# Kernel optimization log

Measured on AMD Instinct MI355X. Metric: run time of the kernel, lower is better.

## Reference

```python
import jax, jax.numpy as jnp
import numpy as np

T = 40          # self.T / timestep
T_REDUCE = 32
FAC = T_REDUCE / T - 0.001  # 0.799, threshold used by create_spike_input_cuda


def conv_t(x, w, b, pad):
    # x: (N,C,H,W,T); w: (O,I,3,3). SLAYER/catSNN conv = Conv3d with time-kernel 1,
    # i.e. the same 2D conv applied independently at every timestep.
    out = jax.lax.conv_general_dilated(
        x, w[..., None], window_strides=(1, 1, 1),
        padding=[(pad, pad), (pad, pad), (0, 0)],
        dimension_numbers=("NCHWT", "OIHWT", "NCHWT"))
    return out + b[None, :, None, None, None]


def avgpool2(x):
    # 2x2 spatial average pool per timestep (snn.pool(2))
    N, C, H, W, Tt = x.shape
    return x.reshape(N, C, H // 2, 2, W // 2, 2, Tt).mean(axis=(3, 5))


def get_spikes(x, thr):
    # catCuda.getSpikes: integrate-and-fire over the last (time) axis with
    # soft reset (subtract threshold). thr broadcastable to x[..., 0].
    xT = jnp.moveaxis(x, -1, 0)                      # (T, N, C, H, W)
    thr_b = jnp.broadcast_to(jnp.asarray(thr, x.dtype), xT.shape[1:])
    def step(v, xt):
        v = v + xt
        s = (v >= thr_b).astype(x.dtype)
        return v - s * thr_b, s
    _, s = jax.lax.scan(step, jnp.zeros(xT.shape[1:], x.dtype), xT)
    return jnp.moveaxis(s, 0, -1)


def requant(y):
    # create_spike_input_cuda(sum(y, time)/T, T): stack the time-mean T times
    # and spike-generate with threshold FAC.
    ym = jnp.mean(y, axis=-1)                        # sum over time / T
    yb = jnp.broadcast_to(ym[..., None], ym.shape + (T,))
    return get_spikes(yb, FAC)


def tts(xi, yi, thr):
    # threshold_training_snn: per-channel spiking of xi, requantized copy of yi.
    return get_spikes(xi, thr[None, :, None, None]), requant(yi)


def forward(x, thr1, thr2, thr3, thr4, thr5, thr6, thr7, p1, p2, p3, p4,
            w1, b1, w2, b2, w3, b3, w4, b4, w5, b5, w6, b6, w7, b7, wc, bc):
    c = conv_t(x, w1, b1, 1)
    xs, ys = tts(c, c, thr1)
    xs, ys = tts(conv_t(xs, w2, b2, 1), conv_t(ys, w2, b2, 1), thr2)
    xs, ys = tts(avgpool2(xs), avgpool2(ys), p1)
    xs, ys = tts(conv_t(xs, w3, b3, 1), conv_t(ys, w3, b3, 1), thr3)
    xs, ys = tts(conv_t(xs, w4, b4, 1), conv_t(ys, w4, b4, 1), thr4)
    xs, ys = tts(avgpool2(xs), avgpool2(ys), p2)
    xs, ys = tts(conv_t(xs, w5, b5, 1), conv_t(ys, w5, b5, 1), thr5)
    xs, ys = tts(conv_t(xs, w6, b6, 1), conv_t(ys, w6, b6, 1), thr6)
    xs, ys = tts(avgpool2(xs), avgpool2(ys), p3)
    xs, ys = tts(conv_t(xs, w7, b7, 0), conv_t(ys, w7, b7, 0), thr7)
    xs, ys = tts(avgpool2(xs), avgpool2(ys), p4)
    N = xs.shape[0]
    xr = xs.reshape(N, 1024, T)                      # spatial is 1x1 here
    logits = jnp.einsum("nct,oc->not", xr, wc) + bc[None, :, None]
    out = jnp.sum(logits, axis=-1) / T               # sum_spikes / T
    return out.reshape(N, 10, 1, 1)


def setup_inputs() -> dict:
    key = jax.random.key(0)
    ks = jax.random.split(key, 32)
    inp = {}
    inp["x"] = jax.random.uniform(ks[0], (2, 3, 32, 32, T), jnp.float32)
    chans = [(3, 128), (128, 128), (128, 256), (256, 256),
             (256, 512), (512, 512), (512, 1024)]
    for i, (ci, co) in enumerate(chans, 1):
        inp[f"w{i}"] = jax.random.normal(ks[i], (co, ci, 3, 3), jnp.float32) * (2.0 / (ci * 9)) ** 0.5
        inp[f"b{i}"] = jnp.zeros((co,), jnp.float32)
    inp["wc"] = jax.random.normal(ks[8], (10, 1024), jnp.float32) * 0.03
    inp["bc"] = jnp.zeros((10,), jnp.float32)
    thr_dims = {"thr1": 128, "thr2": 128, "p1": 128, "thr3": 256, "thr4": 256,
                "p2": 256, "thr5": 512, "thr6": 512, "p3": 512, "thr7": 1024, "p4": 1024}
    for j, (name, d) in enumerate(thr_dims.items()):
        inp[name] = 0.2 + jax.random.uniform(ks[9 + j], (d,), jnp.float32)
    return inp


def reference(x, thr1, thr2, thr3, thr4, thr5, thr6, thr7, p1, p2, p3, p4,
              w1, b1, w2, b2, w3, b3, w4, b4, w5, b5, w6, b6, w7, b7, wc, bc):
    return forward(x, thr1, thr2, thr3, thr4, thr5, thr6, thr7, p1, p2, p3, p4,
                   w1, b1, w2, b2, w3, b3, w4, b4, w5, b5, w6, b6, w7, b7, wc, bc)
```

## Files before the change

kernel.cpp:

```cpp
#include <hip/hip_runtime.h>


constexpr int NT = 40;

typedef __attribute__((ext_vector_type(8))) short s16x8;
typedef __attribute__((ext_vector_type(4))) float f32x4;

__device__ __forceinline__ float bf2f(unsigned short u) {
    return __uint_as_float(((unsigned)u) << 16);
}

__global__ __launch_bounds__(256) void transpose_w(
    const float* __restrict__ w, float* __restrict__ wt, int CO, int R)
{
    __shared__ float tile[32][33];
    const int r0 = blockIdx.x * 32, c0 = blockIdx.y * 32;
    const int tx = threadIdx.x % 32, ty = threadIdx.x / 32;
#pragma unroll
    for (int k = 0; k < 4; k++) {
        const int co = c0 + ty + k * 8, r = r0 + tx;
        if (co < CO && r < R) tile[ty + k * 8][tx] = w[(size_t)co * R + r];
    }
    __syncthreads();
#pragma unroll
    for (int k = 0; k < 4; k++) {
        const int r = r0 + ty + k * 8, co = c0 + tx;
        if (r < R && co < CO) wt[(size_t)r * CO + co] = tile[tx][ty + k * 8];
    }
}

__global__ __launch_bounds__(320) void conv1_c(
    const float* __restrict__ in, const float* __restrict__ wt,
    const float* __restrict__ bias, float* __restrict__ out)
{
    __shared__ float xs_[27 * NT];
    __shared__ float wl[27 * 128];
    const int sp = blockIdx.x;
    const int ho = sp >> 5, wo = sp & 31;
    const int n = blockIdx.z;
    const int tid = threadIdx.x;
    const int tt = tid >> 5;
    const int cc = tid & 31;

    float4 acc[4];
#pragma unroll
    for (int j = 0; j < 4; j++) {
        const float bv = bias[cc * 4 + j];
        acc[j] = make_float4(bv, bv, bv, bv);
    }
    for (int u = tid; u < 270; u += 320) {
        const int r = u / 10, q = u % 10;
        const int cil = r / 9, k = r % 9;
        const int hi = ho + k / 3 - 1, wi = wo + k % 3 - 1;
        float4 v = make_float4(0.f, 0.f, 0.f, 0.f);
        if ((unsigned)hi < 32u && (unsigned)wi < 32u)
            v = *reinterpret_cast<const float4*>(
                in + ((size_t)((n * 3 + cil) * 1024 + hi * 32 + wi)) * NT + q * 4);
        *reinterpret_cast<float4*>(&xs_[r * NT + q * 4]) = v;
    }
    for (int u = tid; u < 864; u += 320) {
        const int r = u >> 5, j = u & 31;
        *reinterpret_cast<float4*>(&wl[r * 128 + j * 4]) =
            *reinterpret_cast<const float4*>(wt + r * 128 + j * 4);
    }
    __syncthreads();
#pragma unroll
    for (int r = 0; r < 27; ++r) {
        const float4 xv = *reinterpret_cast<const float4*>(&xs_[r * NT + tt * 4]);
        const float4 wv = *reinterpret_cast<const float4*>(&wl[r * 128 + cc * 4]);
        acc[0].x = fmaf(xv.x, wv.x, acc[0].x); acc[0].y = fmaf(xv.y, wv.x, acc[0].y);
        acc[0].z = fmaf(xv.z, wv.x, acc[0].z); acc[0].w = fmaf(xv.w, wv.x, acc[0].w);
        acc[1].x = fmaf(xv.x, wv.y, acc[1].x); acc[1].y = fmaf(xv.y, wv.y, acc[1].y);
        acc[1].z = fmaf(xv.z, wv.y, acc[1].z); acc[1].w = fmaf(xv.w, wv.y, acc[1].w);
        acc[2].x = fmaf(xv.x, wv.z, acc[2].x); acc[2].y = fmaf(xv.y, wv.z, acc[2].y);
        acc[2].z = fmaf(xv.z, wv.z, acc[2].z); acc[2].w = fmaf(xv.w, wv.z, acc[2].w);
        acc[3].x = fmaf(xv.x, wv.w, acc[3].x); acc[3].y = fmaf(xv.y, wv.w, acc[3].y);
        acc[3].z = fmaf(xv.z, wv.w, acc[3].z); acc[3].w = fmaf(xv.w, wv.w, acc[3].w);
    }
    const size_t base = (size_t)(n * 1024 + sp) * (NT * 128);
#pragma unroll
    for (int j = 0; j < 4; j++) {
        const int cb = cc * 4 + j;
        out[base + (tt * 4 + 0) * 128 + cb] = acc[j].x;
        out[base + (tt * 4 + 1) * 128 + cb] = acc[j].y;
        out[base + (tt * 4 + 2) * 128 + cb] = acc[j].z;
        out[base + (tt * 4 + 3) * 128 + cb] = acc[j].w;
    }
}

__global__ void split_w(const float* __restrict__ w,
                        unsigned short* __restrict__ hi, unsigned short* __restrict__ mid,
                        unsigned short* __restrict__ lo, int CO, int CIN_)
{
    const int idx = blockIdx.x * blockDim.x + threadIdx.x;
    if (idx >= CO * CIN_) return;
    const int co = idx / CIN_, ci = idx % CIN_;
    const float* src = w + ((size_t)co * CIN_ + ci) * 9;
#pragma unroll
    for (int k = 0; k < 9; ++k) {
        const float f = src[k];
        const unsigned u = __float_as_uint(f);
        const float fh = __uint_as_float(u & 0xFFFF0000u);
        const float r1 = f - fh;
        const unsigned u1 = __float_as_uint(r1);
        const float fm = __uint_as_float(u1 & 0xFFFF0000u);
        const float r2 = r1 - fm;
        const unsigned u2 = __float_as_uint(r2);
        const size_t dst = ((size_t)k * CO + co) * CIN_ + ci;
        hi[dst] = (unsigned short)(u >> 16);
        mid[dst] = (unsigned short)(u1 >> 16);
        lo[dst] = (unsigned short)(u2 >> 16);
    }
}

template<int CIN_SEG, int COUT, int H, int W, int PAD, int BM, int BN, int NSPLIT>
__global__ __launch_bounds__(256, 2) void conv_mfma(
    const unsigned short* __restrict__ spk,
    const unsigned short* __restrict__ wlo, const unsigned short* __restrict__ wmid,
    const unsigned short* __restrict__ whi,
    const float* __restrict__ bias, float* __restrict__ out)
{
    constexpr int CIN = CIN_SEG * NSPLIT;
    constexpr int HO = PAD ? H : H - 2;
    constexpr int WO = PAD ? W : W - 2;
    constexpr int MROW = WO * NT;
    constexpr int MTILES = (MROW + BM - 1) / BM;
    constexpr int WAVES_N = BN / 32;
    constexpr int KC = CIN_SEG / 64;
    __shared__ unsigned short smem[BM * 64 + 3 * BN * 64];

    const int tid = threadIdx.x;
    const int lane = tid & 63;
    const int wv = tid >> 6;
    const int wm = wv / WAVES_N;
    const int wn = wv % WAVES_N;
    const int lr = lane >> 4;
    const int lc = lane & 15;

    const int bx = blockIdx.x;
    const int ho = bx / MTILES;
    const int m0 = (bx % MTILES) * BM;
    const int co0 = blockIdx.y * BN;
    const int n = blockIdx.z / NSPLIT;
    const int split = blockIdx.z % NSPLIT;

    f32x4 acc[4][2];
#pragma unroll
    for (int mf = 0; mf < 4; ++mf)
#pragma unroll
        for (int nf = 0; nf < 2; ++nf) {
            const float bv = (NSPLIT == 1 || split == 0)
                ? bias[co0 + wn * 32 + nf * 16 + lc] : 0.f;
            acc[mf][nf] = {bv, bv, bv, bv};
        }

    const unsigned short* wp[3] = {wlo, wmid, whi};

    for (int kh = 0; kh < 3; ++kh) {
        const int hirow = ho + kh - PAD;
        if (hirow < 0 || hirow >= H) continue;
        const size_t inrow = (size_t)(n * H + hirow) * (W * NT);
        for (int kw = 0; kw < 3; ++kw) {
            const int kwp = kw - PAD;
            const int khw = kh * 3 + kw;
            for (int kc = 0; kc < KC; ++kc) {
                const int ci0 = split * CIN_SEG + kc * 64;
#pragma unroll
                for (int it = 0; it < BM / 32; ++it) {
                    const int idx = it * 256 + tid;
                    const int r = idx >> 3, b = idx & 7;
                    const int mg = m0 + r + kwp * NT;
                    s16x8 v = {0, 0, 0, 0, 0, 0, 0, 0};
                    if ((m0 + r) < MROW && mg >= 0 && mg < W * NT)
                        v = *(const s16x8*)(spk + (inrow + mg) * CIN + ci0 + b * 8);
                    *(s16x8*)&smem[r * 64 + ((b ^ (r & 7)) << 3)] = v;
                }
#pragma unroll
                for (int s = 0; s < 3; ++s) {
                    const unsigned short* wsrc = wp[s] + ((size_t)(khw * COUT + co0)) * CIN + ci0;
#pragma unroll
                    for (int it = 0; it < BN / 32; ++it) {
                        const int idx = it * 256 + tid;
                        const int r = idx >> 3, b = idx & 7;
                        const s16x8 v = *(const s16x8*)(wsrc + (size_t)r * CIN + b * 8);
                        *(s16x8*)&smem[BM * 64 + s * BN * 64 + r * 64 + ((b ^ (r & 7)) << 3)] = v;
                    }
                }
                __syncthreads();
#pragma unroll
                for (int kcs = 0; kcs < 2; ++kcs) {
                    const int c16 = kcs * 4 + lr;
                    s16x8 af[4];
#pragma unroll
                    for (int mf = 0; mf < 4; ++mf) {
                        const int ra = wm * 64 + mf * 16 + lc;
                        af[mf] = *(const s16x8*)&smem[ra * 64 + ((c16 ^ (ra & 7)) << 3)];
                    }
#pragma unroll
                    for (int s = 0; s < 3; ++s) {
#pragma unroll
                        for (int nf = 0; nf < 2; ++nf) {
                            const int rb = wn * 32 + nf * 16 + lc;
                            const s16x8 bf_ = *(const s16x8*)&smem[BM * 64 + s * BN * 64 + rb * 64 + ((c16 ^ (rb & 7)) << 3)];
#pragma unroll
                            for (int mf = 0; mf < 4; ++mf)
                                acc[mf][nf] = __builtin_amdgcn_mfma_f32_16x16x32_bf16(
                                    af[mf], bf_, acc[mf][nf], 0, 0, 0);
                        }
                    }
                }
                __syncthreads();
            }
        }
    }

    const size_t SLAB = (size_t)2 * HO * WO * NT * COUT;
    float* outp = out + (size_t)split * SLAB + (size_t)(n * HO + ho) * (WO * NT) * COUT;
#pragma unroll
    for (int mf = 0; mf < 4; ++mf) {
        const int mbase = m0 + wm * 64 + mf * 16;
        if (mbase >= MROW) continue;
#pragma unroll
        for (int nf = 0; nf < 2; ++nf) {
            const int col = co0 + wn * 32 + nf * 16 + lc;
#pragma unroll
            for (int j = 0; j < 4; ++j) {
                const int m = mbase + lr * 4 + j;
                outp[(size_t)m * COUT + col] = acc[mf][nf][j];
            }
        }
    }
}

__global__ void if_ci(const float* __restrict__ in, unsigned short* __restrict__ spk,
                      const float* __restrict__ thr, int C, int total)
{
    const int idx = blockIdx.x * blockDim.x + threadIdx.x;
    if (idx >= total) return;
    const int c = idx % C;
    const size_t base = (size_t)(idx / C) * NT * C + c;
    const float th = thr[c];
    float v = 0.f;
#pragma unroll
    for (int t = 0; t < NT; ++t) {
        const float x = in[base + (size_t)t * C];
        v += x;
        const float s = (v >= th) ? 1.f : 0.f;
        v -= s * th;
        spk[base + (size_t)t * C] = s != 0.f ? (unsigned short)0x3F80 : (unsigned short)0;
    }
}

__global__ void pool_ci(const unsigned short* __restrict__ in, unsigned short* __restrict__ out,
                        const float* __restrict__ thr, int C, int HO, int WO, int total)
{
    const int idx = blockIdx.x * blockDim.x + threadIdx.x;
    if (idx >= total) return;
    const int c = idx % C;
    const int sp = idx / C;
    const int wo = sp % WO;
    const int ho = (sp / WO) % HO;
    const int n = sp / (WO * HO);
    const int H = 2 * HO, W = 2 * WO;
    const size_t b00 = (((size_t)(n * H + 2 * ho) * W + 2 * wo) * NT) * C + c;
    const size_t oB = (((size_t)(n * HO + ho) * WO + wo) * NT) * C + c;
    const size_t dW = (size_t)NT * C, dH = (size_t)W * NT * C;
    const float th = thr[c];
    float v = 0.f;
#pragma unroll
    for (int t = 0; t < NT; ++t) {
        const size_t o = (size_t)t * C;
        const float a = bf2f(in[b00 + o]) + bf2f(in[b00 + dW + o]) +
                        bf2f(in[b00 + dH + o]) + bf2f(in[b00 + dH + dW + o]);
        v += a * 0.25f;
        const float s = (v >= th) ? 1.f : 0.f;
        v -= s * th;
        out[oB + o] = s != 0.f ? (unsigned short)0x3F80 : (unsigned short)0;
    }
}

__global__ void reduce_if7(const float* __restrict__ part, unsigned short* __restrict__ out,
                           const float* __restrict__ thr, int total)
{
    const int idx = blockIdx.x * blockDim.x + threadIdx.x;
    if (idx >= total) return;
    const int c = idx & 1023;
    const size_t base = (size_t)(idx >> 10) * NT * 1024 + c;
    const size_t SL = 327680;
    const float th = thr[c];
    float v = 0.f;
#pragma unroll
    for (int t = 0; t < NT; ++t) {
        const size_t o = (size_t)t * 1024;
        const float x = part[base + o] + part[SL + base + o] +
                        part[2 * SL + base + o] + part[3 * SL + base + o];
        v += x;
        const float s = (v >= th) ? 1.f : 0.f;
        v -= s * th;
        out[base + o] = s != 0.f ? (unsigned short)0x3F80 : (unsigned short)0;
    }
}

__global__ __launch_bounds__(1024) void classifier_ci(
    const unsigned short* __restrict__ s, const float* __restrict__ wc,
    const float* __restrict__ bc, float* __restrict__ out)
{
    __shared__ float cnt[2][1024];
    const int c = threadIdx.x;
    for (int n = 0; n < 2; n++) {
        float sum = 0.f;
#pragma unroll
        for (int t = 0; t < NT; ++t) sum += bf2f(s[(size_t)(n * NT + t) * 1024 + c]);
        cnt[n][c] = sum;
    }
    __syncthreads();
    if (threadIdx.x < 20) {
        const int n = threadIdx.x / 10, o = threadIdx.x % 10;
        float a = 0.f;
        for (int k = 0; k < 1024; k++) a += cnt[n][k] * wc[o * 1024 + k];
        out[n * 10 + o] = a * (1.f / 40.f) + bc[o];
    }
}

extern "C" void kernel_launch(void* const* d_in, const int* in_sizes, int n_in,
                              void* d_out, int out_size, void* d_ws, size_t ws_size,
                              hipStream_t stream)
{
    const float* x   = (const float*)d_in[0];
    const float* w1  = (const float*)d_in[1];  const float* b1 = (const float*)d_in[2];
    const float* w2  = (const float*)d_in[3];  const float* b2 = (const float*)d_in[4];
    const float* w3  = (const float*)d_in[5];  const float* b3 = (const float*)d_in[6];
    const float* w4  = (const float*)d_in[7];  const float* b4 = (const float*)d_in[8];
    const float* w5  = (const float*)d_in[9];  const float* b5 = (const float*)d_in[10];
    const float* w6  = (const float*)d_in[11]; const float* b6 = (const float*)d_in[12];
    const float* w7  = (const float*)d_in[13]; const float* b7 = (const float*)d_in[14];
    const float* wc  = (const float*)d_in[15]; const float* bc = (const float*)d_in[16];
    const float* thr1 = (const float*)d_in[17];
    const float* thr2 = (const float*)d_in[18];
    const float* p1   = (const float*)d_in[19];
    const float* thr3 = (const float*)d_in[20];
    const float* thr4 = (const float*)d_in[21];
    const float* p2   = (const float*)d_in[22];
    const float* thr5 = (const float*)d_in[23];
    const float* thr6 = (const float*)d_in[24];
    const float* p3   = (const float*)d_in[25];
    const float* thr7 = (const float*)d_in[26];
    const float* p4   = (const float*)d_in[27];

    char* W0 = (char*)d_ws;
    float* OUT = (float*)W0;
    unsigned short* SPKA = (unsigned short*)(W0 + ((size_t)44 << 20));
    unsigned short* SPKB = (unsigned short*)(W0 + ((size_t)66 << 20));
    unsigned short* WH   = (unsigned short*)(W0 + ((size_t)88 << 20));
    unsigned short* WMID = WH + 4718592;
    unsigned short* WLO  = WH + 2 * 4718592;
    float* WT1 = (float*)(W0 + ((size_t)118 << 20));
    float* O = (float*)d_out;

    transpose_w<<<dim3(1, 4), 256, 0, stream>>>(w1, WT1, 128, 27);
    conv1_c<<<dim3(1024, 1, 2), 320, 0, stream>>>(x, WT1, b1, OUT);
    if_ci<<<1024, 256, 0, stream>>>(OUT, SPKA, thr1, 128, 262144);

    split_w<<<64, 256, 0, stream>>>(w2, WH, WMID, WLO, 128, 128);
    conv_mfma<128, 128, 32, 32, 1, 128, 64, 1><<<dim3(320, 2, 2), 256, 0, stream>>>(SPKA, WLO, WMID, WH, b2, OUT);
    if_ci<<<1024, 256, 0, stream>>>(OUT, SPKB, thr2, 128, 262144);
    pool_ci<<<256, 256, 0, stream>>>(SPKB, SPKA, p1, 128, 16, 16, 65536);

    split_w<<<128, 256, 0, stream>>>(w3, WH, WMID, WLO, 256, 128);
    conv_mfma<128, 256, 16, 16, 1, 128, 64, 1><<<dim3(80, 4, 2), 256, 0, stream>>>(SPKA, WLO, WMID, WH, b3, OUT);
    if_ci<<<512, 256, 0, stream>>>(OUT, SPKB, thr3, 256, 131072);

    split_w<<<256, 256, 0, stream>>>(w4, WH, WMID, WLO, 256, 256);
    conv_mfma<256, 256, 16, 16, 1, 128, 64, 1><<<dim3(80, 4, 2), 256, 0, stream>>>(SPKB, WLO, WMID, WH, b4, OUT);
    if_ci<<<512, 256, 0, stream>>>(OUT, SPKA, thr4, 256, 131072);
    pool_ci<<<128, 256, 0, stream>>>(SPKA, SPKB, p2, 256, 8, 8, 32768);

    split_w<<<512, 256, 0, stream>>>(w5, WH, WMID, WLO, 512, 256);
    conv_mfma<256, 512, 8, 8, 1, 64, 128, 1><<<dim3(40, 4, 2), 256, 0, stream>>>(SPKB, WLO, WMID, WH, b5, OUT);
    if_ci<<<256, 256, 0, stream>>>(OUT, SPKA, thr5, 512, 65536);

    split_w<<<1024, 256, 0, stream>>>(w6, WH, WMID, WLO, 512, 512);
    conv_mfma<512, 512, 8, 8, 1, 64, 128, 1><<<dim3(40, 4, 2), 256, 0, stream>>>(SPKA, WLO, WMID, WH, b6, OUT);
    if_ci<<<256, 256, 0, stream>>>(OUT, SPKB, thr6, 512, 65536);
    pool_ci<<<64, 256, 0, stream>>>(SPKB, SPKA, p3, 512, 4, 4, 16384);

    split_w<<<2048, 256, 0, stream>>>(w7, WH, WMID, WLO, 1024, 512);
    conv_mfma<128, 1024, 4, 4, 0, 64, 128, 4><<<dim3(4, 8, 8), 256, 0, stream>>>(SPKA, WLO, WMID, WH, b7, OUT);
    reduce_if7<<<32, 256, 0, stream>>>(OUT, SPKB, thr7, 8192);
    pool_ci<<<8, 256, 0, stream>>>(SPKB, SPKA, p4, 1024, 1, 1, 2048);

    classifier_ci<<<1, 1024, 0, stream>>>(SPKA, wc, bc, O);
}
```

Measured before the change: 562.3 us.

## Merge batch images per block, remap grid for XCD locality, retune conv tiles

The conv kernel becomes conv_mfma2 with a 1D grid. Block indices are remapped so that consecutive tiles land on the same XCD among 8, which should improve L2 reuse of weights and inputs. For the large layers, both batch images are handled in one block (NMERGE=2), so each weight tile loaded into LDS is reused twice. The deeper layers switch to BN=64 with a higher occupancy hint to get more blocks. The cost is more LDS and registers per block for the merged layers, and a possible loss of parallelism.

```diff
diff --git a/kernel.cpp b/kernel.cpp
--- a/kernel.cpp
+++ b/kernel.cpp
@@ -113,8 +113,9 @@
     }
 }
 
-template<int CIN_SEG, int COUT, int H, int W, int PAD, int BM, int BN, int NSPLIT>
-__global__ __launch_bounds__(256, 2) void conv_mfma(
+template<int CIN_SEG, int COUT, int H, int W, int PAD, int BM, int BN,
+         int NSPLIT, int NMERGE, int MINW, bool ZOUT>
+__global__ __launch_bounds__(256, MINW) void conv_mfma2(
     const unsigned short* __restrict__ spk,
     const unsigned short* __restrict__ wlo, const unsigned short* __restrict__ wmid,
     const unsigned short* __restrict__ whi,
@@ -125,55 +126,73 @@
     constexpr int WO = PAD ? W : W - 2;
     constexpr int MROW = WO * NT;
     constexpr int MTILES = (MROW + BM - 1) / BM;
-    constexpr int WAVES_N = BN / 32;
+    constexpr int NX = HO * MTILES;
+    constexpr int NY = COUT / BN;
+    constexpr int NZ = (2 / NMERGE) * NSPLIT;
+    constexpr int NB = NX * NY * NZ;
+    static_assert(NB % 8 == 0, "grid must be divisible by 8 XCDs");
+    constexpr int Q = NB / 8;
     constexpr int KC = CIN_SEG / 64;
-    __shared__ unsigned short smem[BM * 64 + 3 * BN * 64];
+    constexpr int WM = BM / 2;
+    constexpr int MFRAG = WM / 16;
+    __shared__ unsigned short smem[NMERGE * BM * 64 + 3 * BN * 64];
+
+    const int g = blockIdx.x;
+    const int orig = (g % 8) * Q + g / 8;
+    const int x = orig % NX;
+    const int rest = orig / NX;
+    const int y  = ZOUT ? (rest % NY) : (rest / NZ);
+    const int z  = ZOUT ? (rest / NY) : (rest % NZ);
+    const int split = z % NSPLIT;
+    const int nI    = z / NSPLIT;
 
     const int tid = threadIdx.x;
     const int lane = tid & 63;
     const int wv = tid >> 6;
-    const int wm = wv / WAVES_N;
-    const int wn = wv % WAVES_N;
+    const int wm = wv >> 1;
+    const int wn = wv & 1;
     const int lr = lane >> 4;
     const int lc = lane & 15;
 
-    const int bx = blockIdx.x;
-    const int ho = bx / MTILES;
-    const int m0 = (bx % MTILES) * BM;
-    const int co0 = blockIdx.y * BN;
-    const int n = blockIdx.z / NSPLIT;
-    const int split = blockIdx.z % NSPLIT;
-
-    f32x4 acc[4][2];
-#pragma unroll
-    for (int mf = 0; mf < 4; ++mf)
-#pragma unroll
-        for (int nf = 0; nf < 2; ++nf) {
-            const float bv = (NSPLIT == 1 || split == 0)
-                ? bias[co0 + wn * 32 + nf * 16 + lc] : 0.f;
-            acc[mf][nf] = {bv, bv, bv, bv};
-        }
+    const int ho = x / MTILES;
+    const int m0 = (x % MTILES) * BM;
+    const int co0 = y * BN;
+
+    f32x4 acc[NMERGE][MFRAG][2];
+#pragma unroll
+    for (int ni = 0; ni < NMERGE; ++ni)
+#pragma unroll
+        for (int mf = 0; mf < MFRAG; ++mf)
+#pragma unroll
+            for (int nf = 0; nf < 2; ++nf) {
+                const float bv = (NSPLIT == 1 || split == 0)
+                    ? bias[co0 + wn * 32 + nf * 16 + lc] : 0.f;
+                acc[ni][mf][nf] = {bv, bv, bv, bv};
+            }
 
     const unsigned short* wp[3] = {wlo, wmid, whi};
 
     for (int kh = 0; kh < 3; ++kh) {
         const int hirow = ho + kh - PAD;
         if (hirow < 0 || hirow >= H) continue;
-        const size_t inrow = (size_t)(n * H + hirow) * (W * NT);
         for (int kw = 0; kw < 3; ++kw) {
             const int kwp = kw - PAD;
             const int khw = kh * 3 + kw;
             for (int kc = 0; kc < KC; ++kc) {
                 const int ci0 = split * CIN_SEG + kc * 64;
 #pragma unroll
-                for (int it = 0; it < BM / 32; ++it) {
+                for (int it = 0; it < NMERGE * BM / 32; ++it) {
                     const int idx = it * 256 + tid;
-                    const int r = idx >> 3, b = idx & 7;
+                    const int nn = idx / (BM * 8);
+                    const int r = (idx >> 3) % BM, b = idx & 7;
+                    const int n = (NMERGE == 2) ? nn : nI;
                     const int mg = m0 + r + kwp * NT;
                     s16x8 v = {0, 0, 0, 0, 0, 0, 0, 0};
                     if ((m0 + r) < MROW && mg >= 0 && mg < W * NT)
-                        v = *(const s16x8*)(spk + (inrow + mg) * CIN + ci0 + b * 8);
-                    *(s16x8*)&smem[r * 64 + ((b ^ (r & 7)) << 3)] = v;
+                        v = *(const s16x8*)(spk +
+                            ((size_t)(n * H + hirow) * (W * NT) + mg) * CIN + ci0 + b * 8);
+                    const int R = nn * BM + r;
+                    *(s16x8*)&smem[R * 64 + ((b ^ (R & 7)) << 3)] = v;
                 }
 #pragma unroll
                 for (int s = 0; s < 3; ++s) {
@@ -183,29 +202,33 @@
                         const int idx = it * 256 + tid;
                         const int r = idx >> 3, b = idx & 7;
                         const s16x8 v = *(const s16x8*)(wsrc + (size_t)r * CIN + b * 8);
-                        *(s16x8*)&smem[BM * 64 + s * BN * 64 + r * 64 + ((b ^ (r & 7)) << 3)] = v;
+                        *(s16x8*)&smem[NMERGE * BM * 64 + s * BN * 64 + r * 64 + ((b ^ (r & 7)) << 3)] = v;
                     }
                 }
                 __syncthreads();
 #pragma unroll
                 for (int kcs = 0; kcs < 2; ++kcs) {
                     const int c16 = kcs * 4 + lr;
-                    s16x8 af[4];
-#pragma unroll
-                    for (int mf = 0; mf < 4; ++mf) {
-                        const int ra = wm * 64 + mf * 16 + lc;
-                        af[mf] = *(const s16x8*)&smem[ra * 64 + ((c16 ^ (ra & 7)) << 3)];
-                    }
+                    s16x8 af[NMERGE][MFRAG];
+#pragma unroll
+                    for (int ni = 0; ni < NMERGE; ++ni)
+#pragma unroll
+                        for (int mf = 0; mf < MFRAG; ++mf) {
+                            const int Ra = ni * BM + wm * WM + mf * 16 + lc;
+                            af[ni][mf] = *(const s16x8*)&smem[Ra * 64 + ((c16 ^ (Ra & 7)) << 3)];
+                        }
 #pragma unroll
                     for (int s = 0; s < 3; ++s) {
 #pragma unroll
                         for (int nf = 0; nf < 2; ++nf) {
-                            const int rb = wn * 32 + nf * 16 + lc;
-                            const s16x8 bf_ = *(const s16x8*)&smem[BM * 64 + s * BN * 64 + rb * 64 + ((c16 ^ (rb & 7)) << 3)];
-#pragma unroll
-                            for (int mf = 0; mf < 4; ++mf)
-                                acc[mf][nf] = __builtin_amdgcn_mfma_f32_16x16x32_bf16(
-                                    af[mf], bf_, acc[mf][nf], 0, 0, 0);
+                            const int Rb = wn * 32 + nf * 16 + lc;
+                            const s16x8 bf_ = *(const s16x8*)&smem[NMERGE * BM * 64 + s * BN * 64 + Rb * 64 + ((c16 ^ (Rb & 7)) << 3)];
+#pragma unroll
+                            for (int ni = 0; ni < NMERGE; ++ni)
+#pragma unroll
+                                for (int mf = 0; mf < MFRAG; ++mf)
+                                    acc[ni][mf][nf] = __builtin_amdgcn_mfma_f32_16x16x32_bf16(
+                                        af[ni][mf], bf_, acc[ni][mf][nf], 0, 0, 0);
                         }
                     }
                 }
@@ -215,18 +238,22 @@
     }
 
     const size_t SLAB = (size_t)2 * HO * WO * NT * COUT;
-    float* outp = out + (size_t)split * SLAB + (size_t)(n * HO + ho) * (WO * NT) * COUT;
-#pragma unroll
-    for (int mf = 0; mf < 4; ++mf) {
-        const int mbase = m0 + wm * 64 + mf * 16;
-        if (mbase >= MROW) continue;
-#pragma unroll
-        for (int nf = 0; nf < 2; ++nf) {
-            const int col = co0 + wn * 32 + nf * 16 + lc;
-#pragma unroll
-            for (int j = 0; j < 4; ++j) {
-                const int m = mbase + lr * 4 + j;
-                outp[(size_t)m * COUT + col] = acc[mf][nf][j];
+#pragma unroll
+    for (int ni = 0; ni < NMERGE; ++ni) {
+        const int n = (NMERGE == 2) ? ni : nI;
+        float* outp = out + (size_t)split * SLAB + (size_t)(n * HO + ho) * (WO * NT) * COUT;
+#pragma unroll
+        for (int mf = 0; mf < MFRAG; ++mf) {
+            const int mbase = m0 + wm * WM + mf * 16;
+            if (mbase >= MROW) continue;
+#pragma unroll
+            for (int nf = 0; nf < 2; ++nf) {
+                const int col = co0 + wn * 32 + nf * 16 + lc;
+#pragma unroll
+                for (int j = 0; j < 4; ++j) {
+                    const int m = mbase + lr * 4 + j;
+                    outp[(size_t)m * COUT + col] = acc[ni][mf][nf][j];
+                }
             }
         }
     }
@@ -362,30 +389,36 @@
     if_ci<<<1024, 256, 0, stream>>>(OUT, SPKA, thr1, 128, 262144);
 
     split_w<<<64, 256, 0, stream>>>(w2, WH, WMID, WLO, 128, 128);
-    conv_mfma<128, 128, 32, 32, 1, 128, 64, 1><<<dim3(320, 2, 2), 256, 0, stream>>>(SPKA, WLO, WMID, WH, b2, OUT);
+    conv_mfma2<128, 128, 32, 32, 1, 128, 64, 1, 2, 2, true>
+        <<<640, 256, 0, stream>>>(SPKA, WLO, WMID, WH, b2, OUT);
     if_ci<<<1024, 256, 0, stream>>>(OUT, SPKB, thr2, 128, 262144);
     pool_ci<<<256, 256, 0, stream>>>(SPKB, SPKA, p1, 128, 16, 16, 65536);
 
     split_w<<<128, 256, 0, stream>>>(w3, WH, WMID, WLO, 256, 128);
-    conv_mfma<128, 256, 16, 16, 1, 128, 64, 1><<<dim3(80, 4, 2), 256, 0, stream>>>(SPKA, WLO, WMID, WH, b3, OUT);
+    conv_mfma2<128, 256, 16, 16, 1, 128, 64, 1, 2, 2, true>
+        <<<320, 256, 0, stream>>>(SPKA, WLO, WMID, WH, b3, OUT);
     if_ci<<<512, 256, 0, stream>>>(OUT, SPKB, thr3, 256, 131072);
 
     split_w<<<256, 256, 0, stream>>>(w4, WH, WMID, WLO, 256, 256);
-    conv_mfma<256, 256, 16, 16, 1, 128, 64, 1><<<dim3(80, 4, 2), 256, 0, stream>>>(SPKB, WLO, WMID, WH, b4, OUT);
+    conv_mfma2<256, 256, 16, 16, 1, 128, 64, 1, 2, 2, true>
+        <<<320, 256, 0, stream>>>(SPKB, WLO, WMID, WH, b4, OUT);
     if_ci<<<512, 256, 0, stream>>>(OUT, SPKA, thr4, 256, 131072);
     pool_ci<<<128, 256, 0, stream>>>(SPKA, SPKB, p2, 256, 8, 8, 32768);
 
     split_w<<<512, 256, 0, stream>>>(w5, WH, WMID, WLO, 512, 256);
-    conv_mfma<256, 512, 8, 8, 1, 64, 128, 1><<<dim3(40, 4, 2), 256, 0, stream>>>(SPKB, WLO, WMID, WH, b5, OUT);
+    conv_mfma2<256, 512, 8, 8, 1, 64, 64, 1, 1, 4, true>
+        <<<640, 256, 0, stream>>>(SPKB, WLO, WMID, WH, b5, OUT);
     if_ci<<<256, 256, 0, stream>>>(OUT, SPKA, thr5, 512, 65536);
 
     split_w<<<1024, 256, 0, stream>>>(w6, WH, WMID, WLO, 512, 512);
-    conv_mfma<512, 512, 8, 8, 1, 64, 128, 1><<<dim3(40, 4, 2), 256, 0, stream>>>(SPKA, WLO, WMID, WH, b6, OUT);
+    conv_mfma2<512, 512, 8, 8, 1, 64, 64, 1, 1, 4, true>
+        <<<640, 256, 0, stream>>>(SPKA, WLO, WMID, WH, b6, OUT);
     if_ci<<<256, 256, 0, stream>>>(OUT, SPKB, thr6, 512, 65536);
     pool_ci<<<64, 256, 0, stream>>>(SPKB, SPKA, p3, 512, 4, 4, 16384);
 
     split_w<<<2048, 256, 0, stream>>>(w7, WH, WMID, WLO, 1024, 512);
-    conv_mfma<128, 1024, 4, 4, 0, 64, 128, 4><<<dim3(4, 8, 8), 256, 0, stream>>>(SPKA, WLO, WMID, WH, b7, OUT);
+    conv_mfma2<128, 1024, 4, 4, 0, 64, 64, 4, 1, 4, false>
+        <<<512, 256, 0, stream>>>(SPKA, WLO, WMID, WH, b7, OUT);
     reduce_if7<<<32, 256, 0, stream>>>(OUT, SPKB, thr7, 8192);
     pool_ci<<<8, 256, 0, stream>>>(SPKB, SPKA, p4, 1024, 1, 1, 2048);
 
```

Result: slower. 592.8 us (+5.4%).

## Restructure conv into padded-input double-buffered direct-to-LDS pipeline with XCD-aware block mapping

Applied to the files above, without the earlier changes.

Replaces the conv kernel with a version that reads from explicitly zero-padded spike buffers, so the boundary checks go away. It stages A and B tiles straight into LDS with global_load_lds, double-buffered across the 9*KC chunks with a single barrier per chunk. Each block now processes both images at once, sharing the weight tiles, and uses 64x64 tiles. Block indices are remapped so consecutive work lands on the same XCD. Additional halo_zero kernels and padded-layout variants of the if/pool kernels add launches, and the 80KB of dynamic LDS may limit occupancy.

```diff
diff --git a/kernel.cpp b/kernel.cpp
--- a/kernel.cpp
+++ b/kernel.cpp
@@ -9,6 +9,10 @@
 __device__ __forceinline__ float bf2f(unsigned short u) {
     return __uint_as_float(((unsigned)u) << 16);
 }
+
+#define GLOAD16(gp, lp) __builtin_amdgcn_global_load_lds(                      \
+    (const __attribute__((address_space(1))) void*)(gp),                       \
+    (__attribute__((address_space(3))) void*)(lp), 16, 0, 0)
 
 __global__ __launch_bounds__(256) void transpose_w(
     const float* __restrict__ w, float* __restrict__ wt, int CO, int R)
@@ -113,146 +117,169 @@
     }
 }
 
-template<int CIN_SEG, int COUT, int H, int W, int PAD, int BM, int BN, int NSPLIT>
-__global__ __launch_bounds__(256, 2) void conv_mfma(
+template<int CIN_SEG, int COUT, int HP, int WP, int NSPLIT>
+__global__ __launch_bounds__(256, 2) void conv_p(
     const unsigned short* __restrict__ spk,
     const unsigned short* __restrict__ wlo, const unsigned short* __restrict__ wmid,
     const unsigned short* __restrict__ whi,
     const float* __restrict__ bias, float* __restrict__ out)
 {
     constexpr int CIN = CIN_SEG * NSPLIT;
-    constexpr int HO = PAD ? H : H - 2;
-    constexpr int WO = PAD ? W : W - 2;
+    constexpr int HO = HP - 2, WO = WP - 2;
     constexpr int MROW = WO * NT;
-    constexpr int MTILES = (MROW + BM - 1) / BM;
-    constexpr int WAVES_N = BN / 32;
+    constexpr int MTILES = (MROW + 63) / 64;
     constexpr int KC = CIN_SEG / 64;
-    __shared__ unsigned short smem[BM * 64 + 3 * BN * 64];
+    constexpr int NCHUNK = 9 * KC;
+    constexpr int NX = HO * MTILES;
+    constexpr int NY = COUT / 64;
+    constexpr int NB = NX * NY * NSPLIT;
+    static_assert(NB % 8 == 0, "grid must divide across 8 XCDs");
+    constexpr int Q = NB / 8;
+    constexpr int ASH = 2 * 64 * 64;
+    constexpr int BUFSH = ASH + 3 * 64 * 64;
+    constexpr size_t SLAB = (size_t)2 * HO * WO * NT * COUT;
+
+    extern __shared__ unsigned short smem_raw[];
+
+    const int g = blockIdx.x;
+    const int orig = (g & 7) * Q + (g >> 3);
+    const int split = orig % NSPLIT;
+    const int x = (orig / NSPLIT) % NX;
+    const int y = orig / (NSPLIT * NX);
+    const int ho = x / MTILES;
+    const int m0 = (x % MTILES) * 64;
+    const int co0 = y * 64;
 
     const int tid = threadIdx.x;
     const int lane = tid & 63;
     const int wv = tid >> 6;
-    const int wm = wv / WAVES_N;
-    const int wn = wv % WAVES_N;
-    const int lr = lane >> 4;
-    const int lc = lane & 15;
-
-    const int bx = blockIdx.x;
-    const int ho = bx / MTILES;
-    const int m0 = (bx % MTILES) * BM;
-    const int co0 = blockIdx.y * BN;
-    const int n = blockIdx.z / NSPLIT;
-    const int split = blockIdx.z % NSPLIT;
-
-    f32x4 acc[4][2];
-#pragma unroll
-    for (int mf = 0; mf < 4; ++mf)
-#pragma unroll
-        for (int nf = 0; nf < 2; ++nf) {
-            const float bv = (NSPLIT == 1 || split == 0)
-                ? bias[co0 + wn * 32 + nf * 16 + lc] : 0.f;
-            acc[mf][nf] = {bv, bv, bv, bv};
+    const int wm = wv >> 1, wn = wv & 1;
+    const int lr = lane >> 4, lc = lane & 15;
+    const size_t laneoff = (size_t)(lane >> 3) * CIN + (size_t)((((lane & 7) ^ ((lane >> 3) & 7))) << 3);
+
+    f32x4 acc[2][2][2];
+#pragma unroll
+    for (int img = 0; img < 2; ++img)
+#pragma unroll
+        for (int mf = 0; mf < 2; ++mf)
+#pragma unroll
+            for (int nf = 0; nf < 2; ++nf) {
+                const float bv = (NSPLIT == 1 || split == 0)
+                    ? bias[co0 + wn * 32 + nf * 16 + lc] : 0.f;
+                acc[img][mf][nf] = {bv, bv, bv, bv};
+            }
+
+    auto stage = [&](int buf, int c) {
+        const int kh = c / (3 * KC);
+        const int rem = c - kh * 3 * KC;
+        const int kw = rem / KC;
+        const int kc = rem - kw * KC;
+        const int ci0 = split * CIN_SEG + kc * 64;
+        const int khw = kh * 3 + kw;
+        unsigned short* lbase = smem_raw + (size_t)buf * BUFSH;
+#pragma unroll
+        for (int s = 0; s < 10; ++s) {
+            const int slot = wv * 10 + s;
+            const unsigned short* gp;
+            int lofs;
+            if (slot < 16) {
+                const int img = slot >> 3;
+                const int r0 = (slot & 7) << 3;
+                const size_t rowpos = (size_t)((img * HP + ho + kh) * WP) * NT
+                                      + (size_t)(m0 + kw * NT + r0);
+                gp = spk + rowpos * CIN + ci0 + laneoff;
+                lofs = (img * 64 + r0) * 64;
+            } else {
+                const int si = slot - 16;
+                const int sp_ = si >> 3;
+                const int r0 = (si & 7) << 3;
+                const unsigned short* wb = (sp_ == 0) ? wlo : ((sp_ == 1) ? wmid : whi);
+                gp = wb + ((size_t)(khw * COUT + co0) + r0) * CIN + ci0 + laneoff;
+                lofs = ASH + (sp_ * 64 + r0) * 64;
+            }
+            GLOAD16(gp, lbase + lofs);
         }
-
-    const unsigned short* wp[3] = {wlo, wmid, whi};
-
-    for (int kh = 0; kh < 3; ++kh) {
-        const int hirow = ho + kh - PAD;
-        if (hirow < 0 || hirow >= H) continue;
-        const size_t inrow = (size_t)(n * H + hirow) * (W * NT);
-        for (int kw = 0; kw < 3; ++kw) {
-            const int kwp = kw - PAD;
-            const int khw = kh * 3 + kw;
-            for (int kc = 0; kc < KC; ++kc) {
-                const int ci0 = split * CIN_SEG + kc * 64;
-#pragma unroll
-                for (int it = 0; it < BM / 32; ++it) {
-                    const int idx = it * 256 + tid;
-                    const int r = idx >> 3, b = idx & 7;
-                    const int mg = m0 + r + kwp * NT;
-                    s16x8 v = {0, 0, 0, 0, 0, 0, 0, 0};
-                    if ((m0 + r) < MROW && mg >= 0 && mg < W * NT)
-                        v = *(const s16x8*)(spk + (inrow + mg) * CIN + ci0 + b * 8);
-                    *(s16x8*)&smem[r * 64 + ((b ^ (r & 7)) << 3)] = v;
+    };
+
+    auto compute = [&](int buf) {
+        const unsigned short* sb = smem_raw + (size_t)buf * BUFSH;
+#pragma unroll
+        for (int kcs = 0; kcs < 2; ++kcs) {
+            const int c16 = kcs * 4 + lr;
+            s16x8 af[2][2];
+#pragma unroll
+            for (int img = 0; img < 2; ++img)
+#pragma unroll
+                for (int mf = 0; mf < 2; ++mf) {
+                    const int Ra = img * 64 + wm * 32 + mf * 16 + lc;
+                    af[img][mf] = *(const s16x8*)&sb[Ra * 64 + ((c16 ^ (Ra & 7)) << 3)];
                 }
 #pragma unroll
-                for (int s = 0; s < 3; ++s) {
-                    const unsigned short* wsrc = wp[s] + ((size_t)(khw * COUT + co0)) * CIN + ci0;
-#pragma unroll
-                    for (int it = 0; it < BN / 32; ++it) {
-                        const int idx = it * 256 + tid;
-                        const int r = idx >> 3, b = idx & 7;
-                        const s16x8 v = *(const s16x8*)(wsrc + (size_t)r * CIN + b * 8);
-                        *(s16x8*)&smem[BM * 64 + s * BN * 64 + r * 64 + ((b ^ (r & 7)) << 3)] = v;
-                    }
+            for (int s = 0; s < 3; ++s) {
+#pragma unroll
+                for (int nf = 0; nf < 2; ++nf) {
+                    const int Rb = wn * 32 + nf * 16 + lc;
+                    const s16x8 bq = *(const s16x8*)&sb[ASH + s * 4096 + Rb * 64 + ((c16 ^ (Rb & 7)) << 3)];
+#pragma unroll
+                    for (int img = 0; img < 2; ++img)
+#pragma unroll
+                        for (int mf = 0; mf < 2; ++mf)
+                            acc[img][mf][nf] = __builtin_amdgcn_mfma_f32_16x16x32_bf16(
+                                af[img][mf], bq, acc[img][mf][nf], 0, 0, 0);
                 }
-                __syncthreads();
-#pragma unroll
-                for (int kcs = 0; kcs < 2; ++kcs) {
-                    const int c16 = kcs * 4 + lr;
-                    s16x8 af[4];
-#pragma unroll
-                    for (int mf = 0; mf < 4; ++mf) {
-                        const int ra = wm * 64 + mf * 16 + lc;
-                        af[mf] = *(const s16x8*)&smem[ra * 64 + ((c16 ^ (ra & 7)) << 3)];
-                    }
-#pragma unroll
-                    for (int s = 0; s < 3; ++s) {
-#pragma unroll
-                        for (int nf = 0; nf < 2; ++nf) {
-                            const int rb = wn * 32 + nf * 16 + lc;
-                            const s16x8 bf_ = *(const s16x8*)&smem[BM * 64 + s * BN * 64 + rb * 64 + ((c16 ^ (rb & 7)) << 3)];
-#pragma unroll
-                            for (int mf = 0; mf < 4; ++mf)
-                                acc[mf][nf] = __builtin_amdgcn_mfma_f32_16x16x32_bf16(
-                                    af[mf], bf_, acc[mf][nf], 0, 0, 0);
-                        }
-                    }
-                }
-                __syncthreads();
             }
         }
-    }
-
-    const size_t SLAB = (size_t)2 * HO * WO * NT * COUT;
-    float* outp = out + (size_t)split * SLAB + (size_t)(n * HO + ho) * (WO * NT) * COUT;
-#pragma unroll
-    for (int mf = 0; mf < 4; ++mf) {
-        const int mbase = m0 + wm * 64 + mf * 16;
-        if (mbase >= MROW) continue;
-#pragma unroll
-        for (int nf = 0; nf < 2; ++nf) {
-            const int col = co0 + wn * 32 + nf * 16 + lc;
-#pragma unroll
-            for (int j = 0; j < 4; ++j) {
-                const int m = mbase + lr * 4 + j;
-                outp[(size_t)m * COUT + col] = acc[mf][nf][j];
+    };
+
+    stage(0, 0);
+    asm volatile("s_waitcnt vmcnt(0)" ::: "memory");
+    __builtin_amdgcn_s_barrier();
+    __builtin_amdgcn_sched_barrier(0);
+    for (int c = 0; c < NCHUNK; ++c) {
+        const int cur = c & 1;
+        if (c + 1 < NCHUNK) stage(cur ^ 1, c + 1);
+        compute(cur);
+        asm volatile("s_waitcnt vmcnt(0)" ::: "memory");
+        __builtin_amdgcn_s_barrier();
+        __builtin_amdgcn_sched_barrier(0);
+    }
+
+#pragma unroll
+    for (int img = 0; img < 2; ++img) {
+        float* outp = out + split * SLAB + ((size_t)(img * HO + ho) * WO * NT) * COUT;
+#pragma unroll
+        for (int mf = 0; mf < 2; ++mf) {
+            const int mbase = m0 + wm * 32 + mf * 16;
+            if (mbase >= MROW) continue;
+#pragma unroll
+            for (int nf = 0; nf < 2; ++nf) {
+                const int col = co0 + wn * 32 + nf * 16 + lc;
+#pragma unroll
+                for (int j = 0; j < 4; ++j) {
+                    const int m = mbase + lr * 4 + j;
+                    outp[(size_t)m * COUT + col] = acc[img][mf][nf][j];
+                }
             }
         }
     }
 }
 
+__global__ void halo_zero(unsigned short* __restrict__ buf, int HP, int WP, int TC)
+{
+    const int cell = blockIdx.x, n = blockIdx.y;
+    int h, w;
+    if (cell < WP)            { h = 0;       w = cell; }
+    else if (cell < 2 * WP)   { h = HP - 1;  w = cell - WP; }
+    else { const int s = cell - 2 * WP; h = 1 + (s >> 1); w = (s & 1) ? (WP - 1) : 0; }
+    unsigned short* p = buf + (((size_t)(n * HP + h) * WP) + w) * TC;
+    const s16x8 z = {0, 0, 0, 0, 0, 0, 0, 0};
+    for (int i = threadIdx.x * 8; i < TC; i += blockDim.x * 8)
+        *(s16x8*)(p + i) = z;
+}
+
 __global__ void if_ci(const float* __restrict__ in, unsigned short* __restrict__ spk,
-                      const float* __restrict__ thr, int C, int total)
-{
-    const int idx = blockIdx.x * blockDim.x + threadIdx.x;
-    if (idx >= total) return;
-    const int c = idx % C;
-    const size_t base = (size_t)(idx / C) * NT * C + c;
-    const float th = thr[c];
-    float v = 0.f;
-#pragma unroll
-    for (int t = 0; t < NT; ++t) {
-        const float x = in[base + (size_t)t * C];
-        v += x;
-        const float s = (v >= th) ? 1.f : 0.f;
-        v -= s * th;
-        spk[base + (size_t)t * C] = s != 0.f ? (unsigned short)0x3F80 : (unsigned short)0;
-    }
-}
-
-__global__ void pool_ci(const unsigned short* __restrict__ in, unsigned short* __restrict__ out,
-                        const float* __restrict__ thr, int C, int HO, int WO, int total)
+                      const float* __restrict__ thr, int C, int HO, int WO,
+                      int HP, int WP, int off, int total)
 {
     const int idx = blockIdx.x * blockDim.x + threadIdx.x;
     if (idx >= total) return;
@@ -261,21 +288,44 @@
     const int wo = sp % WO;
     const int ho = (sp / WO) % HO;
     const int n = sp / (WO * HO);
-    const int H = 2 * HO, W = 2 * WO;
-    const size_t b00 = (((size_t)(n * H + 2 * ho) * W + 2 * wo) * NT) * C + c;
-    const size_t oB = (((size_t)(n * HO + ho) * WO + wo) * NT) * C + c;
-    const size_t dW = (size_t)NT * C, dH = (size_t)W * NT * C;
     const float th = thr[c];
+    const size_t ib = (size_t)sp * NT * C + c;
+    const size_t ob = (((size_t)(n * HP + ho + off) * WP) + wo + off) * NT * C + c;
+    float v = 0.f;
+#pragma unroll
+    for (int t = 0; t < NT; ++t) {
+        v += in[ib + (size_t)t * C];
+        const float s = (v >= th) ? 1.f : 0.f;
+        v -= s * th;
+        spk[ob + (size_t)t * C] = (s != 0.f) ? (unsigned short)0x3F80 : (unsigned short)0;
+    }
+}
+
+__global__ void pool_ci(const unsigned short* __restrict__ in, unsigned short* __restrict__ out,
+                        const float* __restrict__ thr, int C, int HO, int WO,
+                        int IHP, int IWP, int offi, int OHP, int OWP, int offo, int total)
+{
+    const int idx = blockIdx.x * blockDim.x + threadIdx.x;
+    if (idx >= total) return;
+    const int c = idx % C;
+    const int sp = idx / C;
+    const int wo = sp % WO;
+    const int ho = (sp / WO) % HO;
+    const int n = sp / (WO * HO);
+    const float th = thr[c];
+    const size_t i00 = (((size_t)(n * IHP + 2 * ho + offi) * IWP) + 2 * wo + offi) * NT * C + c;
+    const size_t dW = (size_t)NT * C, dH = (size_t)IWP * NT * C;
+    const size_t ob = (((size_t)(n * OHP + ho + offo) * OWP) + wo + offo) * NT * C + c;
     float v = 0.f;
 #pragma unroll
     for (int t = 0; t < NT; ++t) {
         const size_t o = (size_t)t * C;
-        const float a = bf2f(in[b00 + o]) + bf2f(in[b00 + dW + o]) +
-                        bf2f(in[b00 + dH + o]) + bf2f(in[b00 + dH + dW + o]);
+        const float a = bf2f(in[i00 + o]) + bf2f(in[i00 + dW + o]) +
+                        bf2f(in[i00 + dH + o]) + bf2f(in[i00 + dH + dW + o]);
         v += a * 0.25f;
         const float s = (v >= th) ? 1.f : 0.f;
         v -= s * th;
-        out[oB + o] = s != 0.f ? (unsigned short)0x3F80 : (unsigned short)0;
+        out[ob + o] = (s != 0.f) ? (unsigned short)0x3F80 : (unsigned short)0;
     }
 }
 
@@ -297,7 +347,7 @@
         v += x;
         const float s = (v >= th) ? 1.f : 0.f;
         v -= s * th;
-        out[base + o] = s != 0.f ? (unsigned short)0x3F80 : (unsigned short)0;
+        out[base + o] = (s != 0.f) ? (unsigned short)0x3F80 : (unsigned short)0;
     }
 }
 
@@ -349,45 +399,56 @@
 
     char* W0 = (char*)d_ws;
     float* OUT = (float*)W0;
-    unsigned short* SPKA = (unsigned short*)(W0 + ((size_t)44 << 20));
-    unsigned short* SPKB = (unsigned short*)(W0 + ((size_t)66 << 20));
-    unsigned short* WH   = (unsigned short*)(W0 + ((size_t)88 << 20));
-    unsigned short* WMID = WH + 4718592;
-    unsigned short* WLO  = WH + 2 * 4718592;
-    float* WT1 = (float*)(W0 + ((size_t)118 << 20));
+    unsigned short* WH   = (unsigned short*)(W0 + (40ull << 20));
+    unsigned short* WMID = (unsigned short*)(W0 + (49ull << 20));
+    unsigned short* WLO  = (unsigned short*)(W0 + (58ull << 20));
+    unsigned short* R1   = (unsigned short*)(W0 + (67ull << 20));
+    unsigned short* R2   = (unsigned short*)(W0 + (90ull << 20));
+    unsigned short* R3   = (unsigned short*)(W0 + (97ull << 20));
+    float* WT1 = (float*)(W0 + (117ull << 20));
+    unsigned short* S1 = R1, *S3 = R1, *S5 = R1;
+    unsigned short* S2 = R2, *S4 = R2, *S6 = R2;
+    unsigned short* U2 = R3, *U4 = R3, *U6 = R3;
+    unsigned short* S7 = R3;
+    unsigned short* P4 = (unsigned short*)((char*)R3 + (2ull << 20));
     float* O = (float*)d_out;
 
     transpose_w<<<dim3(1, 4), 256, 0, stream>>>(w1, WT1, 128, 27);
     conv1_c<<<dim3(1024, 1, 2), 320, 0, stream>>>(x, WT1, b1, OUT);
-    if_ci<<<1024, 256, 0, stream>>>(OUT, SPKA, thr1, 128, 262144);
+    halo_zero<<<dim3(132, 2), 256, 0, stream>>>(S1, 34, 34, 5120);
+    if_ci<<<1024, 256, 0, stream>>>(OUT, S1, thr1, 128, 32, 32, 34, 34, 1, 262144);
 
     split_w<<<64, 256, 0, stream>>>(w2, WH, WMID, WLO, 128, 128);
-    conv_mfma<128, 128, 32, 32, 1, 128, 64, 1><<<dim3(320, 2, 2), 256, 0, stream>>>(SPKA, WLO, WMID, WH, b2, OUT);
-    if_ci<<<1024, 256, 0, stream>>>(OUT, SPKB, thr2, 128, 262144);
-    pool_ci<<<256, 256, 0, stream>>>(SPKB, SPKA, p1, 128, 16, 16, 65536);
+    conv_p<128, 128, 34, 34, 1><<<1280, 256, 81920, stream>>>(S1, WLO, WMID, WH, b2, OUT);
+    if_ci<<<1024, 256, 0, stream>>>(OUT, U2, thr2, 128, 32, 32, 32, 32, 0, 262144);
+    halo_zero<<<dim3(68, 2), 256, 0, stream>>>(S2, 18, 18, 5120);
+    pool_ci<<<256, 256, 0, stream>>>(U2, S2, p1, 128, 16, 16, 32, 32, 0, 18, 18, 1, 65536);
 
     split_w<<<128, 256, 0, stream>>>(w3, WH, WMID, WLO, 256, 128);
-    conv_mfma<128, 256, 16, 16, 1, 128, 64, 1><<<dim3(80, 4, 2), 256, 0, stream>>>(SPKA, WLO, WMID, WH, b3, OUT);
-    if_ci<<<512, 256, 0, stream>>>(OUT, SPKB, thr3, 256, 131072);
+    conv_p<128, 256, 18, 18, 1><<<640, 256, 81920, stream>>>(S2, WLO, WMID, WH, b3, OUT);
+    halo_zero<<<dim3(68, 2), 256, 0, stream>>>(S3, 18, 18, 10240);
+    if_ci<<<512, 256, 0, stream>>>(OUT, S3, thr3, 256, 16, 16, 18, 18, 1, 131072);
 
     split_w<<<256, 256, 0, stream>>>(w4, WH, WMID, WLO, 256, 256);
-    conv_mfma<256, 256, 16, 16, 1, 128, 64, 1><<<dim3(80, 4, 2), 256, 0, stream>>>(SPKB, WLO, WMID, WH, b4, OUT);
-    if_ci<<<512, 256, 0, stream>>>(OUT, SPKA, thr4, 256, 131072);
-    pool_ci<<<128, 256, 0, stream>>>(SPKA, SPKB, p2, 256, 8, 8, 32768);
+    conv_p<256, 256, 18, 18, 1><<<640, 256, 81920, stream>>>(S3, WLO, WMID, WH, b4, OUT);
+    if_ci<<<512, 256, 0, stream>>>(OUT, U4, thr4, 256, 16, 16, 16, 16, 0, 131072);
+    halo_zero<<<dim3(36, 2), 256, 0, stream>>>(S4, 10, 10, 10240);
+    pool_ci<<<128, 256, 0, stream>>>(U4, S4, p2, 256, 8, 8, 16, 16, 0, 10, 10, 1, 32768);
 
     split_w<<<512, 256, 0, stream>>>(w5, WH, WMID, WLO, 512, 256);
-    conv_mfma<256, 512, 8, 8, 1, 64, 128, 1><<<dim3(40, 4, 2), 256, 0, stream>>>(SPKB, WLO, WMID, WH, b5, OUT);
-    if_ci<<<256, 256, 0, stream>>>(OUT, SPKA, thr5, 512, 65536);
+    conv_p<256, 512, 10, 10, 1><<<320, 256, 81920, stream>>>(S4, WLO, WMID, WH, b5, OUT);
+    halo_zero<<<dim3(36, 2), 256, 0, stream>>>(S5, 10, 10, 20480);
+    if_ci<<<256, 256, 0, stream>>>(OUT, S5, thr5, 512, 8, 8, 10, 10, 1, 65536);
 
     split_w<<<1024, 256, 0, stream>>>(w6, WH, WMID, WLO, 512, 512);
-    conv_mfma<512, 512, 8, 8, 1, 64, 128, 1><<<dim3(40, 4, 2), 256, 0, stream>>>(SPKA, WLO, WMID, WH, b6, OUT);
-    if_ci<<<256, 256, 0, stream>>>(OUT, SPKB, thr6, 512, 65536);
-    pool_ci<<<64, 256, 0, stream>>>(SPKB, SPKA, p3, 512, 4, 4, 16384);
+    conv_p<512, 512, 10, 10, 1><<<320, 256, 81920, stream>>>(S5, WLO, WMID, WH, b6, OUT);
+    if_ci<<<256, 256, 0, stream>>>(OUT, U6, thr6, 512, 8, 8, 8, 8, 0, 65536);
+    pool_ci<<<64, 256, 0, stream>>>(U6, S6, p3, 512, 4, 4, 8, 8, 0, 4, 4, 0, 16384);
 
     split_w<<<2048, 256, 0, stream>>>(w7, WH, WMID, WLO, 1024, 512);
-    conv_mfma<128, 1024, 4, 4, 0, 64, 128, 4><<<dim3(4, 8, 8), 256, 0, stream>>>(SPKA, WLO, WMID, WH, b7, OUT);
-    reduce_if7<<<32, 256, 0, stream>>>(OUT, SPKB, thr7, 8192);
-    pool_ci<<<8, 256, 0, stream>>>(SPKB, SPKA, p4, 1024, 1, 1, 2048);
-
-    classifier_ci<<<1, 1024, 0, stream>>>(SPKA, wc, bc, O);
-}
+    conv_p<128, 1024, 4, 4, 4><<<256, 256, 81920, stream>>>(S6, WLO, WMID, WH, b7, OUT);
+    reduce_if7<<<32, 256, 0, stream>>>(OUT, S7, thr7, 8192);
+    pool_ci<<<8, 256, 0, stream>>>(S7, P4, p4, 1024, 1, 1, 2, 2, 0, 1, 1, 0, 2048);
+
+    classifier_ci<<<1, 1024, 0, stream>>>(P4, wc, bc, O);
+}
```

After: 1.991 ms. 3.54x slower.
